# Kernel optimization log

Hardware: AMD Instinct MI355X
Metric: run time of the kernel (lower is better)

The kernel has to match this reference:

```python
import jax, jax.numpy as jnp
import numpy as np


def setup_inputs() -> dict:
    key = jax.random.key(0)
    k1, k2, k3, k4 = jax.random.split(key, 4)
    B, T, C, H = 32, 2048, 384, 64
    x = jax.random.normal(k1, (B, T, C), dtype=jnp.float32)
    # nn.Linear(C, H, bias=False): weight stored [H, C], applied as x @ W.T.
    # We store the transposed [C, H] form directly.
    s = 1.0 / np.sqrt(C)
    Wk = jax.random.normal(k2, (C, H), dtype=jnp.float32) * s
    Wq = jax.random.normal(k3, (C, H), dtype=jnp.float32) * s
    Wv = jax.random.normal(k4, (C, H), dtype=jnp.float32) * s
    return {"x": x, "Wk": Wk, "Wq": Wq, "Wv": Wv}


def reference(x, Wk, Wq, Wv):
    # x: [B, T, C]; Wk/Wq/Wv: [C, H]
    T = x.shape[1]
    H = Wk.shape[1]
    k = jnp.einsum('btc,ch->bth', x, Wk)
    q = jnp.einsum('btc,ch->bth', x, Wq)
    v = jnp.einsum('btc,ch->bth', x, Wv)
    scale = H ** (-0.5)
    scores = jnp.einsum('bth,bsh->bts', q, k) * scale  # [B, T, T]
    causal = jnp.tril(jnp.ones((T, T), dtype=bool))
    scores = jnp.where(causal, scores, -jnp.inf)
    attn = jax.nn.softmax(scores, axis=-1)
    # dropout is identity in eval mode
    out = jnp.einsum('bts,bsh->bth', attn, v)  # [B, T, H]
    return out
```

## Files before the change

### kernel.cpp

```cpp
#include <hip/hip_runtime.h>

typedef __bf16 bf16_8 __attribute__((ext_vector_type(8)));
typedef __bf16 bf16_4 __attribute__((ext_vector_type(4)));
typedef float  f32x4  __attribute__((ext_vector_type(4)));

#define NB 32
#define NT 2048
#define NC 384
#define NH 64

static __device__ __forceinline__ f32x4 mfma16(bf16_8 a, bf16_8 b, f32x4 c) {
  return __builtin_amdgcn_mfma_f32_16x16x32_bf16(a, b, c, 0, 0, 0);
}

__global__ void pack_w_kernel(const float* __restrict__ Wk, const float* __restrict__ Wq,
                              const float* __restrict__ Wv, __bf16* __restrict__ Wt) {
  int idx = blockIdx.x * 256 + threadIdx.x;
  if (idx >= 192 * NC) return;
  int n = idx / NC, k = idx % NC;
  int sel = n >> 6, h = n & 63;
  const float* W = (sel == 0) ? Wq : (sel == 1 ? Wk : Wv);
  float v = W[k * NH + h];
  if (sel == 0) v *= 0.125f * 1.44269504088896f;
  Wt[idx] = (__bf16)v;
}

__launch_bounds__(1024, 4)
__global__ void qkv_kernel(const float* __restrict__ x, const __bf16* __restrict__ Wt,
                           __bf16* __restrict__ Q, __bf16* __restrict__ K,
                           __bf16* __restrict__ Vt) {
  __shared__ __bf16 Wl[192 * 384];

  const int tid  = threadIdx.x;
  const int lane = tid & 63, wq = tid >> 6;
  const int quad = lane >> 4, l16 = lane & 15;
  const int rowblk = blockIdx.x * 256;
  const int rbase  = rowblk + wq * 16;
  const int row    = rbase + l16;

  #pragma unroll
  for (int i = 0; i < 9; ++i) {
    int g = tid + i * 1024;
    int r = g / 48, c = g - r * 48;
    int p = c ^ (r & 7);
    uint4 v = ((const uint4*)Wt)[g];
    *(uint4*)&Wl[(r * 48 + p) * 8] = v;
  }
  __syncthreads();

  f32x4 acc[12];
  #pragma unroll
  for (int n = 0; n < 12; ++n) acc[n] = f32x4{0.f, 0.f, 0.f, 0.f};

  const float* xrow = x + (size_t)row * NC;
  f32x4 xp0[4], xp1[4];
  #pragma unroll
  for (int d = 0; d < 4; ++d) {
    xp0[d] = *(const f32x4*)(xrow + d * 32 + quad * 8);
    xp1[d] = *(const f32x4*)(xrow + d * 32 + quad * 8 + 4);
  }

  #pragma unroll
  for (int kc = 0; kc < 12; ++kc) {
    const int slot = kc & 3;
    bf16_8 a;
    a[0] = (__bf16)xp0[slot][0]; a[1] = (__bf16)xp0[slot][1];
    a[2] = (__bf16)xp0[slot][2]; a[3] = (__bf16)xp0[slot][3];
    a[4] = (__bf16)xp1[slot][0]; a[5] = (__bf16)xp1[slot][1];
    a[6] = (__bf16)xp1[slot][2]; a[7] = (__bf16)xp1[slot][3];
    if (kc + 4 < 12) {
      const float* xp = xrow + (kc + 4) * 32 + quad * 8;
      xp0[slot] = *(const f32x4*)xp;
      xp1[slot] = *(const f32x4*)(xp + 4);
    }
    const int pc = (kc * 4 + quad) ^ (l16 & 7);
    const int cbase = l16 * 48 + pc;
    #pragma unroll
    for (int n = 0; n < 12; ++n) {
      bf16_8 b = *(const bf16_8*)&Wl[(n * 16 * 48 + cbase) * 8];
      acc[n] = mfma16(a, b, acc[n]);
    }
  }

  #pragma unroll
  for (int n = 0; n < 8; ++n)
    #pragma unroll
    for (int r = 0; r < 4; ++r) {
      int orow = rbase + quad * 4 + r;
      int h = (n & 3) * 16 + l16;
      __bf16 bv = (__bf16)acc[n][r];
      if (n < 4) Q[(size_t)orow * NH + h] = bv;
      else       K[(size_t)orow * NH + h] = bv;
    }

  __syncthreads();
  __bf16 (*Vl)[264] = (__bf16(*)[264])Wl;
  #pragma unroll
  for (int n = 8; n < 12; ++n) {
    int h = (n - 8) * 16 + l16;
    int t0 = wq * 16 + quad * 4;
    bf16_4 p;
    p[0] = (__bf16)acc[n][0]; p[1] = (__bf16)acc[n][1];
    p[2] = (__bf16)acc[n][2]; p[3] = (__bf16)acc[n][3];
    *(bf16_4*)&Vl[h][t0] = p;
  }
  __syncthreads();
  {
    int h = tid >> 4, seg = tid & 15;
    int bb = rowblk >> 11, t0 = (rowblk & (NT - 1)) + seg * 16;
    const __bf16* src = &Vl[h][seg * 16];
    __bf16* dst = Vt + ((size_t)(bb * NH + h)) * NT + t0;
    ((uint4*)dst)[0] = ((const uint4*)src)[0];
    ((uint4*)dst)[1] = ((const uint4*)src)[1];
  }
}

__launch_bounds__(512, 2)
__global__ void attn_kernel(const __bf16* __restrict__ Q, const __bf16* __restrict__ K,
                            const __bf16* __restrict__ Vt, float* __restrict__ out) {
  __shared__ __bf16 Ks[128][72];
  __shared__ __bf16 Vs[64][136];
  __shared__ __bf16 Ps[8][16][136];

  const int tid  = threadIdx.x;
  const int lane = tid & 63, wq = tid >> 6;
  const int quad = lane >> 4, l16 = lane & 15;
  const int b    = blockIdx.x >> 3;
  const int pair = blockIdx.x & 7;

  const float NEG_INF = -__builtin_inff();
  const int kr = tid >> 2, kc = (tid & 3) * 16;
  const int vr = tid >> 3, vc = (tid & 7) * 16;
  const __bf16* Kg = K  + (size_t)b * NT * NH;
  const __bf16* Vg = Vt + (size_t)b * NH * NT;

  for (int pass = 0; pass < 2; ++pass) {
    const int jpos = pass ? pair : (15 - pair);
    const int q0 = jpos * 128;
    const int nSuper = jpos + 1;

    const __bf16* qrow = Q + ((size_t)(b * NT + q0 + wq * 16 + l16)) * NH + quad * 8;
    bf16_8 qf0 = *(const bf16_8*)qrow;
    bf16_8 qf1 = *(const bf16_8*)(qrow + 32);

    f32x4 o[4];
    #pragma unroll
    for (int i = 0; i < 4; ++i) o[i] = f32x4{0.f, 0.f, 0.f, 0.f};
    float m_i = NEG_INF, l_i = 0.f;

    {
      const uint4* kp = (const uint4*)(Kg + (size_t)kr * NH + kc);
      uint4 k0 = kp[0], k1 = kp[1];
      const uint4* vp = (const uint4*)(Vg + (size_t)vr * NT + vc);
      uint4 v0 = vp[0], v1 = vp[1];
      *(uint4*)&Ks[kr][kc]     = k0; *(uint4*)&Ks[kr][kc + 8] = k1;
      *(uint4*)&Vs[vr][vc]     = v0; *(uint4*)&Vs[vr][vc + 8] = v1;
    }

    for (int i = 0; i < nSuper; ++i) {
      const bool more = (i + 1 < nSuper);
      const bool diag = (i == nSuper - 1);
      uint4 pk[2], pv[2];
      if (more) {
        const int s0n = (i + 1) * 128;
        const uint4* kp = (const uint4*)(Kg + (size_t)(s0n + kr) * NH + kc);
        pk[0] = kp[0]; pk[1] = kp[1];
        const uint4* vp = (const uint4*)(Vg + (size_t)vr * NT + s0n + vc);
        pv[0] = vp[0]; pv[1] = vp[1];
      }
      __syncthreads();

      const int stMax = diag ? (wq + 1) : 8;
      f32x4 sv[8];
      #pragma unroll
      for (int st = 0; st < 8; ++st) {
        if (st < stMax) {
          bf16_8 a0 = *(const bf16_8*)&Ks[st * 16 + l16][quad * 8];
          bf16_8 a1 = *(const bf16_8*)&Ks[st * 16 + l16][quad * 8 + 32];
          f32x4 accv = f32x4{0.f, 0.f, 0.f, 0.f};
          accv = mfma16(a0, qf0, accv);
          accv = mfma16(a1, qf1, accv);
          sv[st] = accv;
        } else {
          sv[st] = f32x4{NEG_INF, NEG_INF, NEG_INF, NEG_INF};
        }
      }

      if (diag) {
        int slimit = wq * 16 + l16;
        #pragma unroll
        for (int st = 0; st < 8; ++st)
          if (st < stMax)
            #pragma unroll
            for (int rr = 0; rr < 4; ++rr) {
              int sloc = st * 16 + quad * 4 + rr;
              if (sloc > slimit) sv[st][rr] = NEG_INF;
            }
      }

      float mx = NEG_INF;
      #pragma unroll
      for (int st = 0; st < 8; ++st)
        #pragma unroll
        for (int rr = 0; rr < 4; ++rr) mx = fmaxf(mx, sv[st][rr]);
      mx = fmaxf(mx, __shfl_xor(mx, 16));
      mx = fmaxf(mx, __shfl_xor(mx, 32));
      float m_new = fmaxf(m_i, mx);
      float alpha = __builtin_amdgcn_exp2f(m_i - m_new);

      float lsum = 0.f;
      #pragma unroll
      for (int st = 0; st < 8; ++st) {
        bf16_4 pkv;
        #pragma unroll
        for (int rr = 0; rr < 4; ++rr) {
          float p = __builtin_amdgcn_exp2f(sv[st][rr] - m_new);
          lsum += p;
          pkv[rr] = (__bf16)p;
        }
        *(bf16_4*)&Ps[wq][l16][st * 16 + quad * 4] = pkv;
      }
      lsum += __shfl_xor(lsum, 16);
      lsum += __shfl_xor(lsum, 32);
      l_i = l_i * alpha + lsum;
      m_i = m_new;

      f32x4 av;
      #pragma unroll
      for (int rr = 0; rr < 4; ++rr) av[rr] = __shfl(alpha, quad * 4 + rr);
      #pragma unroll
      for (int nt = 0; nt < 4; ++nt)
        #pragma unroll
        for (int rr = 0; rr < 4; ++rr) o[nt][rr] *= av[rr];

      const int cMax = diag ? ((wq >> 1) + 1) : 4;
      #pragma unroll
      for (int c = 0; c < 4; ++c) {
        if (c < cMax) {
          bf16_8 pa = *(const bf16_8*)&Ps[wq][l16][c * 32 + quad * 8];
          #pragma unroll
          for (int nt = 0; nt < 4; ++nt) {
            bf16_8 bv = *(const bf16_8*)&Vs[nt * 16 + l16][c * 32 + quad * 8];
            o[nt] = mfma16(pa, bv, o[nt]);
          }
        }
      }

      __syncthreads();
      if (more) {
        *(uint4*)&Ks[kr][kc]     = pk[0]; *(uint4*)&Ks[kr][kc + 8] = pk[1];
        *(uint4*)&Vs[vr][vc]     = pv[0]; *(uint4*)&Vs[vr][vc + 8] = pv[1];
      }
    }

    f32x4 lv;
    #pragma unroll
    for (int rr = 0; rr < 4; ++rr) lv[rr] = 1.f / __shfl(l_i, quad * 4 + rr);
    float* op = out + ((size_t)(b * NT + q0 + wq * 16 + quad * 4)) * NH + l16;
    #pragma unroll
    for (int nt = 0; nt < 4; ++nt)
      #pragma unroll
      for (int rr = 0; rr < 4; ++rr)
        op[(size_t)rr * NH + nt * 16] = o[nt][rr] * lv[rr];
  }
}

extern "C" void kernel_launch(void* const* d_in, const int* in_sizes, int n_in,
                              void* d_out, int out_size, void* d_ws, size_t ws_size,
                              hipStream_t stream) {
  const float* x  = (const float*)d_in[0];
  const float* Wk = (const float*)d_in[1];
  const float* Wq = (const float*)d_in[2];
  const float* Wv = (const float*)d_in[3];
  float* out = (float*)d_out;

  char* ws = (char*)d_ws;
  __bf16* Wt  = (__bf16*)ws;
  __bf16* Qb  = (__bf16*)(ws + 256 * 1024);
  __bf16* Kb  = Qb + (size_t)NB * NT * NH;
  __bf16* Vtb = Kb + (size_t)NB * NT * NH;

  pack_w_kernel<<<288, 256, 0, stream>>>(Wk, Wq, Wv, Wt);
  qkv_kernel<<<256, 1024, 0, stream>>>(x, Wt, Qb, Kb, Vtb);
  attn_kernel<<<NB * 8, 512, 0, stream>>>(Qb, Kb, Vtb, out);
}
```

Measured before the change: 239.6 us.

## Shrink attention tiles to 64 and double-buffer K/V shared memory

The attention kernel now uses 64-row query and key tiles with 256-thread blocks, launching twice as many blocks (512 instead of 256). K/V tiles are double-buffered in shared memory, so the next tile is stored into the alternate buffer mid-iteration and one barrier per tile is dropped. This aims to fill more CUs, since 256 blocks is close to the CU count, and to overlap loads with compute. In exchange it costs more loop iterations, per-tile overhead and softmax rescaling, and smaller MFMA work per barrier.

```diff
diff --git a/kernel.cpp b/kernel.cpp
--- a/kernel.cpp
+++ b/kernel.cpp
@@ -115,29 +115,28 @@
   }
 }
 
-__launch_bounds__(512, 2)
+__launch_bounds__(256, 2)
 __global__ void attn_kernel(const __bf16* __restrict__ Q, const __bf16* __restrict__ K,
                             const __bf16* __restrict__ Vt, float* __restrict__ out) {
-  __shared__ __bf16 Ks[128][72];
-  __shared__ __bf16 Vs[64][136];
-  __shared__ __bf16 Ps[8][16][136];
+  __shared__ __bf16 Ks[2][64][72];
+  __shared__ __bf16 Vs[2][64][72];
+  __shared__ __bf16 Ps[4][16][72];
 
   const int tid  = threadIdx.x;
   const int lane = tid & 63, wq = tid >> 6;
   const int quad = lane >> 4, l16 = lane & 15;
-  const int b    = blockIdx.x >> 3;
-  const int pair = blockIdx.x & 7;
+  const int b    = blockIdx.x >> 4;
+  const int pr   = blockIdx.x & 15;
 
   const float NEG_INF = -__builtin_inff();
-  const int kr = tid >> 2, kc = (tid & 3) * 16;
-  const int vr = tid >> 3, vc = (tid & 7) * 16;
+  const int sr = tid >> 2, sc = (tid & 3) * 16;
   const __bf16* Kg = K  + (size_t)b * NT * NH;
   const __bf16* Vg = Vt + (size_t)b * NH * NT;
 
   for (int pass = 0; pass < 2; ++pass) {
-    const int jpos = pass ? pair : (15 - pair);
-    const int q0 = jpos * 128;
-    const int nSuper = jpos + 1;
+    const int jpos = pass ? pr : (31 - pr);
+    const int q0 = jpos * 64;
+    const int nT = jpos + 1;
 
     const __bf16* qrow = Q + ((size_t)(b * NT + q0 + wq * 16 + l16)) * NH + quad * 8;
     bf16_8 qf0 = *(const bf16_8*)qrow;
@@ -148,35 +147,37 @@
     for (int i = 0; i < 4; ++i) o[i] = f32x4{0.f, 0.f, 0.f, 0.f};
     float m_i = NEG_INF, l_i = 0.f;
 
+    __syncthreads();
     {
-      const uint4* kp = (const uint4*)(Kg + (size_t)kr * NH + kc);
+      const uint4* kp = (const uint4*)(Kg + (size_t)sr * NH + sc);
       uint4 k0 = kp[0], k1 = kp[1];
-      const uint4* vp = (const uint4*)(Vg + (size_t)vr * NT + vc);
+      const uint4* vp = (const uint4*)(Vg + (size_t)sr * NT + sc);
       uint4 v0 = vp[0], v1 = vp[1];
-      *(uint4*)&Ks[kr][kc]     = k0; *(uint4*)&Ks[kr][kc + 8] = k1;
-      *(uint4*)&Vs[vr][vc]     = v0; *(uint4*)&Vs[vr][vc + 8] = v1;
-    }
-
-    for (int i = 0; i < nSuper; ++i) {
-      const bool more = (i + 1 < nSuper);
-      const bool diag = (i == nSuper - 1);
-      uint4 pk[2], pv[2];
+      *(uint4*)&Ks[0][sr][sc]     = k0; *(uint4*)&Ks[0][sr][sc + 8] = k1;
+      *(uint4*)&Vs[0][sr][sc]     = v0; *(uint4*)&Vs[0][sr][sc + 8] = v1;
+    }
+
+    for (int i = 0; i < nT; ++i) {
+      const int cur = i & 1;
+      const bool more = (i + 1 < nT);
+      const bool diag = (i == nT - 1);
+      uint4 pk0, pk1, pv0, pv1;
       if (more) {
-        const int s0n = (i + 1) * 128;
-        const uint4* kp = (const uint4*)(Kg + (size_t)(s0n + kr) * NH + kc);
-        pk[0] = kp[0]; pk[1] = kp[1];
-        const uint4* vp = (const uint4*)(Vg + (size_t)vr * NT + s0n + vc);
-        pv[0] = vp[0]; pv[1] = vp[1];
+        const int s0n = (i + 1) * 64;
+        const uint4* kp = (const uint4*)(Kg + (size_t)(s0n + sr) * NH + sc);
+        pk0 = kp[0]; pk1 = kp[1];
+        const uint4* vp = (const uint4*)(Vg + (size_t)sr * NT + s0n + sc);
+        pv0 = vp[0]; pv1 = vp[1];
       }
       __syncthreads();
 
-      const int stMax = diag ? (wq + 1) : 8;
-      f32x4 sv[8];
-      #pragma unroll
-      for (int st = 0; st < 8; ++st) {
+      const int stMax = diag ? (wq + 1) : 4;
+      f32x4 sv[4];
+      #pragma unroll
+      for (int st = 0; st < 4; ++st) {
         if (st < stMax) {
-          bf16_8 a0 = *(const bf16_8*)&Ks[st * 16 + l16][quad * 8];
-          bf16_8 a1 = *(const bf16_8*)&Ks[st * 16 + l16][quad * 8 + 32];
+          bf16_8 a0 = *(const bf16_8*)&Ks[cur][st * 16 + l16][quad * 8];
+          bf16_8 a1 = *(const bf16_8*)&Ks[cur][st * 16 + l16][quad * 8 + 32];
           f32x4 accv = f32x4{0.f, 0.f, 0.f, 0.f};
           accv = mfma16(a0, qf0, accv);
           accv = mfma16(a1, qf1, accv);
@@ -189,7 +190,7 @@
       if (diag) {
         int slimit = wq * 16 + l16;
         #pragma unroll
-        for (int st = 0; st < 8; ++st)
+        for (int st = 0; st < 4; ++st)
           if (st < stMax)
             #pragma unroll
             for (int rr = 0; rr < 4; ++rr) {
@@ -200,7 +201,7 @@
 
       float mx = NEG_INF;
       #pragma unroll
-      for (int st = 0; st < 8; ++st)
+      for (int st = 0; st < 4; ++st)
         #pragma unroll
         for (int rr = 0; rr < 4; ++rr) mx = fmaxf(mx, sv[st][rr]);
       mx = fmaxf(mx, __shfl_xor(mx, 16));
@@ -210,7 +211,7 @@
 
       float lsum = 0.f;
       #pragma unroll
-      for (int st = 0; st < 8; ++st) {
+      for (int st = 0; st < 4; ++st) {
         bf16_4 pkv;
         #pragma unroll
         for (int rr = 0; rr < 4; ++rr) {
@@ -225,6 +226,11 @@
       l_i = l_i * alpha + lsum;
       m_i = m_new;
 
+      if (more) {
+        *(uint4*)&Ks[1 - cur][sr][sc]     = pk0; *(uint4*)&Ks[1 - cur][sr][sc + 8] = pk1;
+        *(uint4*)&Vs[1 - cur][sr][sc]     = pv0; *(uint4*)&Vs[1 - cur][sr][sc + 8] = pv1;
+      }
+
       f32x4 av;
       #pragma unroll
       for (int rr = 0; rr < 4; ++rr) av[rr] = __shfl(alpha, quad * 4 + rr);
@@ -233,23 +239,17 @@
         #pragma unroll
         for (int rr = 0; rr < 4; ++rr) o[nt][rr] *= av[rr];
 
-      const int cMax = diag ? ((wq >> 1) + 1) : 4;
-      #pragma unroll
-      for (int c = 0; c < 4; ++c) {
+      const int cMax = diag ? ((wq >> 1) + 1) : 2;
+      #pragma unroll
+      for (int c = 0; c < 2; ++c) {
         if (c < cMax) {
           bf16_8 pa = *(const bf16_8*)&Ps[wq][l16][c * 32 + quad * 8];
           #pragma unroll
           for (int nt = 0; nt < 4; ++nt) {
-            bf16_8 bv = *(const bf16_8*)&Vs[nt * 16 + l16][c * 32 + quad * 8];
+            bf16_8 bv = *(const bf16_8*)&Vs[cur][nt * 16 + l16][c * 32 + quad * 8];
             o[nt] = mfma16(pa, bv, o[nt]);
           }
         }
-      }
-
-      __syncthreads();
-      if (more) {
-        *(uint4*)&Ks[kr][kc]     = pk[0]; *(uint4*)&Ks[kr][kc + 8] = pk[1];
-        *(uint4*)&Vs[vr][vc]     = pv[0]; *(uint4*)&Vs[vr][vc + 8] = pv[1];
       }
     }
 
@@ -282,5 +282,5 @@
 
   pack_w_kernel<<<288, 256, 0, stream>>>(Wk, Wq, Wv, Wt);
   qkv_kernel<<<256, 1024, 0, stream>>>(x, Wt, Qb, Kb, Vtb);
-  attn_kernel<<<NB * 8, 512, 0, stream>>>(Qb, Kb, Vtb, out);
-}
+  attn_kernel<<<NB * 16, 256, 0, stream>>>(Qb, Kb, Vtb, out);
+}
```

After: 212.1 us. -11.5%, faster.
